# Performance work log

Hardware: AMD Instinct MI355X
Metric: run time of the kernel (lower is better)

The kernel has to match this reference:

```python
import jax, jax.numpy as jnp
import numpy as np

B, T, P, D, V = 8, 4096, 4, 512, 256
N = T // P          # 1024 patches (T divisible by P, so no padding needed)
K = 16              # k_retrieval
W = 4               # local message-passing window
H = 8               # refresh attention heads = min(8, D//64)
ROUNDS = 6
EPS = 1e-5


def layer_norm(x, g, b):
    mu = x.mean(-1, keepdims=True)
    var = ((x - mu) ** 2).mean(-1, keepdims=True)
    return (x - mu) / jnp.sqrt(var + EPS) * g + b


def setup_inputs() -> dict:
    key = jax.random.key(0)
    ks = iter(jax.random.split(key, 48))
    w = lambda *s: jax.random.normal(next(ks), s, jnp.float32) * 0.02
    p = {}
    p['x'] = jax.random.randint(next(ks), (B, T), 0, V)
    p['emb'] = w(V, D)
    p['pos_emb'] = w(P, D)
    p['gru_w_ih'] = w(D, 3 * D); p['gru_w_hh'] = w(D, 3 * D)
    p['gru_b_ih'] = jnp.zeros(3 * D); p['gru_b_hh'] = jnp.zeros(3 * D)
    p['patch_ln_g'] = jnp.ones(D); p['patch_ln_b'] = jnp.zeros(D)
    p['summ_w'] = w(D, D); p['summ_b'] = jnp.zeros(D)
    p['msg_w1'] = w(2 * D, D); p['msg_b1'] = jnp.zeros(D)
    p['msg_w2'] = w(D, D); p['msg_b2'] = jnp.zeros(D)
    p['msg_ln_g'] = jnp.ones(D); p['msg_ln_b'] = jnp.zeros(D)
    p['q_w'] = w(D, D); p['q_b'] = jnp.zeros(D)
    p['k_w'] = w(D, D); p['k_b'] = jnp.zeros(D)
    p['v_w'] = w(D, D); p['v_b'] = jnp.zeros(D)
    p['o_w'] = w(D, D); p['o_b'] = jnp.zeros(D)
    p['gc_w_ih'] = w(2 * D, 3 * D); p['gc_w_hh'] = w(D, 3 * D)
    p['gc_b_ih'] = jnp.zeros(3 * D); p['gc_b_hh'] = jnp.zeros(3 * D)
    p['ar_ln_g'] = jnp.ones(D); p['ar_ln_b'] = jnp.zeros(D)
    p['ar_qkv_w'] = w(D, 3 * D); p['ar_qkv_b'] = jnp.zeros(3 * D)
    p['ar_out_w'] = w(D, D); p['ar_out_b'] = jnp.zeros(D)
    p['broad_w'] = w(D, D); p['broad_b'] = jnp.zeros(D)
    p['ln_g'] = jnp.ones(D); p['ln_b'] = jnp.zeros(D)
    p['head_w'] = w(D, V)
    return p


def reference(x, emb, pos_emb, gru_w_ih, gru_w_hh, gru_b_ih, gru_b_hh,
              patch_ln_g, patch_ln_b, summ_w, summ_b,
              msg_w1, msg_b1, msg_w2, msg_b2, msg_ln_g, msg_ln_b,
              q_w, q_b, k_w, k_b, v_w, v_b, o_w, o_b,
              gc_w_ih, gc_w_hh, gc_b_ih, gc_b_hh,
              ar_ln_g, ar_ln_b, ar_qkv_w, ar_qkv_b, ar_out_w, ar_out_b,
              broad_w, broad_b, ln_g, ln_b, head_w):
    # --- patch encoding: embedding + pos + GRU over the P tokens of each patch ---
    flat = x.reshape(B * N, P)
    h = emb[flat] + pos_emb[None, :, :]                      # [B*N, P, D]

    def gru_step(hprev, xt):
        gi = xt @ gru_w_ih + gru_b_ih
        gh = hprev @ gru_w_hh + gru_b_hh
        ir, iz, inn = jnp.split(gi, 3, -1)
        hr, hz, hn = jnp.split(gh, 3, -1)
        r = jax.nn.sigmoid(ir + hr)
        z = jax.nn.sigmoid(iz + hz)
        n = jnp.tanh(inn + r * hn)
        hnew = (1 - z) * n + z * hprev
        return hnew, hnew

    _, hs = jax.lax.scan(gru_step, jnp.zeros((B * N, D), h.dtype), jnp.swapaxes(h, 0, 1))
    local = layer_norm(jnp.swapaxes(hs, 0, 1), patch_ln_g, patch_ln_b).reshape(B, N, P, D)
    h = local.mean(2) @ summ_w + summ_b                      # patch summaries [B, N, D]

    # --- RoPE tables over patch positions ---
    d = D // 2
    inv_freq = 1.0 / (10000.0 ** (jnp.arange(0, D, 2, dtype=jnp.float32) / D))
    freqs = jnp.arange(N, dtype=jnp.float32)[:, None] * inv_freq[None, :]   # [N, d]
    cos, sin = jnp.cos(freqs), jnp.sin(freqs)

    def rotary(t):
        t1, t2 = t[..., :d], t[..., d:]
        return jnp.concatenate([t1 * cos - t2 * sin, t2 * cos + t1 * sin], -1)

    causal = jnp.tril(jnp.ones((N, N), bool))
    hd = D // H

    for rnd in range(ROUNDS):
        # windowed neighbor gather (W past patches + self), fused MLP messages
        padded = jnp.pad(h, ((0, 0), (W, 0), (0, 0)))
        neighbors = jnp.stack([padded[:, W - w:W - w + N] for w in range(W + 1)], 2)  # [B,N,W+1,D]
        self_exp = jnp.broadcast_to(h[:, :, None, :], neighbors.shape)
        msg_in = jnp.concatenate([self_exp, neighbors], -1)
        msgs = (jax.nn.gelu(msg_in @ msg_w1 + msg_b1, approximate=False) @ msg_w2 + msg_b2).mean(2)

        # RoPE top-k sparse causal attention (N > K, sparse branch always taken)
        q = rotary(h @ q_w + q_b)
        k = rotary(h @ k_w + k_b)
        v = h @ v_w + v_b
        scores = jnp.einsum('bnd,bmd->bnm', q, k) / jnp.sqrt(jnp.float32(D))
        scores = jnp.where(causal, scores, -jnp.inf)
        tv, ti = jax.lax.top_k(scores, K)
        probs = jax.nn.softmax(tv, -1)  # == softmax of -inf-filled sparse score matrix
        vg = jax.vmap(lambda vi, ii: vi[ii])(v, ti)          # [B, N, K, D]
        retrieved = jnp.einsum('bnk,bnkd->bnd', probs, vg) @ o_w + o_b

        # GRUCell gated write
        wi = jnp.concatenate([msgs, retrieved], -1)
        gi = wi @ gc_w_ih + gc_b_ih
        gh = h @ gc_w_hh + gc_b_hh
        ir, iz, inn = jnp.split(gi, 3, -1)
        hr, hz, hn = jnp.split(gh, 3, -1)
        r = jax.nn.sigmoid(ir + hr)
        z = jax.nn.sigmoid(iz + hz)
        n = jnp.tanh(inn + r * hn)
        h = layer_norm((1 - z) * n + z * h, msg_ln_g, msg_ln_b)

        # global causal MHA refresh every 2 rounds (eval mode, no dropout)
        if (rnd + 1) % 2 == 0:
            res = h
            hn_ = layer_norm(h, ar_ln_g, ar_ln_b)
            qkv = hn_ @ ar_qkv_w + ar_qkv_b
            qh, kh, vh = [t.reshape(B, N, H, hd) for t in jnp.split(qkv, 3, -1)]
            s = jnp.einsum('bnhd,bmhd->bhnm', qh, kh) / jnp.sqrt(jnp.float32(hd))
            a = jax.nn.softmax(jnp.where(causal, s, -jnp.inf), -1)
            o = jnp.einsum('bhnm,bmhd->bnhd', a, vh).reshape(B, N, D)
            h = res + (o @ ar_out_w + ar_out_b)

    # broadcast patch state back to tokens, project to vocab
    broad = h @ broad_w + broad_b
    final = (local + broad[:, :, None, :]).reshape(B, N * P, D)[:, :T]
    return layer_norm(final, ln_g, ln_b) @ head_w            # [B, T, V]
```

## Files before the change

### kernel.cpp

```cpp
#include <hip/hip_runtime.h>
#include <math.h>

constexpr int CB = 8, CT = 4096, CP = 4, CD = 512, CV = 256;
constexpr int CN = 1024, CK = 16, CH = 8, CHD = 64;
constexpr int ROWS = CB * CN;
constexpr int TROWS = CB * CT;
constexpr float CEPS = 1e-5f;
constexpr size_t PN = (size_t)ROWS * CD;

constexpr size_t OFF_LOCAL = 0;
constexpr size_t OFF_HP    = OFF_LOCAL + (size_t)ROWS * CP * CD;
constexpr size_t OFF_X4    = OFF_HP    + PN;
constexpr size_t OFF_MS    = OFF_X4    + (size_t)ROWS * 2560;
constexpr size_t OFF_A     = OFF_MS    + PN;
constexpr size_t OFF_B     = OFF_A     + PN;
constexpr size_t OFF_BIAS  = OFF_B     + PN;
constexpr size_t OFF_WT    = OFF_BIAS  + 4096;

constexpr size_t TOT_W    = 7471104;
constexpr size_t T_GRU_IH = 0;
constexpr size_t T_GRU_HH = 786432;
constexpr size_t T_SUMM   = 1572864;
constexpr size_t T_FUSE   = 1835008;
constexpr size_t T_MSG2   = 3145728;
constexpr size_t T_OW     = 3407872;
constexpr size_t T_GCAB   = 3670016;
constexpr size_t T_GC_HH  = 5242880;
constexpr size_t T_AR_QKV = 6029312;
constexpr size_t T_AR_OUT = 6815744;
constexpr size_t T_BROAD  = 7077888;
constexpr size_t T_HEAD   = 7340032;

constexpr int F_ACC_F32  = 1;
constexpr int F_ACC_PAIR = 2;
constexpr int F_WR_F32   = 4;
constexpr int F_WR_PAIR  = 8;
constexpr int F_TRI      = 16;
constexpr int F_SPLIT    = 32;

typedef __attribute__((ext_vector_type(8))) short short8;
typedef __attribute__((ext_vector_type(4))) float f32x4;

__device__ __forceinline__ float sigm(float x) { return 1.f / (1.f + expf(-x)); }
__device__ __forceinline__ float geluf(float x) {
  return 0.5f * x * (1.f + erff(x * 0.7071067811865475f));
}
__device__ __forceinline__ unsigned short bf_hi(float x) {
  const unsigned u = __float_as_uint(x);
  return (unsigned short)((u + 0x7FFFu + ((u >> 16) & 1u)) >> 16);
}
__device__ __forceinline__ float bf_f(unsigned short h) {
  return __uint_as_float((unsigned)h << 16);
}
__device__ __forceinline__ void split_store(float v, unsigned short* ph, unsigned short* pl) {
  const unsigned short h = bf_hi(v);
  *ph = h; *pl = bf_hi(v - bf_f(h));
}
__device__ __forceinline__ float blk_sum(float v, float* red) {
#pragma unroll
  for (int o = 32; o > 0; o >>= 1) v += __shfl_down(v, o, 64);
  const int wv = threadIdx.x >> 6, ln = threadIdx.x & 63;
  __syncthreads();
  if (ln == 0) red[wv] = v;
  __syncthreads();
  return red[0] + red[1] + red[2] + red[3];
}

__device__ __forceinline__ int xcd_swz(int i, int n) {
  if (n < 8) return i;
  const int q = n >> 3, r = n & 7;
  const int xcd = i & 7, slot = i >> 3;
  return (xcd < r ? xcd * (q + 1) : r * (q + 1) + (xcd - r) * q) + slot;
}

__global__ __launch_bounds__(256) void transpose_split(const float* __restrict__ in,
                                                       unsigned short* __restrict__ oh,
                                                       unsigned short* __restrict__ ol,
                                                       int K, int N, int ldk, int ko)
{
  __shared__ float tile[32][33];
  const int n0 = blockIdx.x * 32, k0 = blockIdx.y * 32;
  const int tx = threadIdx.x & 31, ty = threadIdx.x >> 5;
#pragma unroll
  for (int i = 0; i < 32; i += 8)
    tile[ty + i][tx] = in[(size_t)(k0 + ty + i) * N + n0 + tx];
  __syncthreads();
#pragma unroll
  for (int i = 0; i < 32; i += 8) {
    const float v = tile[tx][ty + i];
    const unsigned short h = bf_hi(v);
    const size_t o = (size_t)(n0 + ty + i) * ldk + ko + k0 + tx;
    oh[o] = h;
    ol[o] = bf_hi(v - bf_f(h));
  }
}

__global__ void concat_bias5(const float* __restrict__ b1, const float* __restrict__ qb,
                             const float* __restrict__ kb, const float* __restrict__ vb,
                             float* __restrict__ o)
{
  const int i = blockIdx.x * 256 + threadIdx.x;
  float v;
  if (i < 512) v = b1[i];
  else if (i < 1024) v = 0.f;
  else if (i < 1536) v = qb[i - 1024];
  else if (i < 2048) v = kb[i - 1536];
  else v = vb[i - 2048];
  o[i] = v;
}

template <bool P3>
__global__ __launch_bounds__(256, 2) void gemm_bf3(
    const unsigned short* __restrict__ AH, const unsigned short* __restrict__ AL,
    const unsigned short* __restrict__ A2H, const unsigned short* __restrict__ A2L,
    int K1, int lda,
    const unsigned short* __restrict__ BH, const unsigned short* __restrict__ BL, int ldb,
    const float* __restrict__ bias, float scale,
    float* __restrict__ Cf, int ldc, float* __restrict__ Cf2,
    unsigned short* __restrict__ CHp, unsigned short* __restrict__ CLp, int ldcp,
    int K, int flags, long long sA, long long sB, long long sC)
{
  AH += (size_t)blockIdx.z * sA; AL += (size_t)blockIdx.z * sA;
  BH += (size_t)blockIdx.z * sB; BL += (size_t)blockIdx.z * sB;
  if (Cf) Cf += (size_t)blockIdx.z * sC;
  int bm, bn;
  if (flags & F_TRI) {
    int t = xcd_swz(blockIdx.x, gridDim.x), i = 0, acc = 0;
    while (acc + i + 1 <= t) { ++i; acc += i; }
    bm = i << 7; bn = (t - acc) << 7;
  } else {
    const int w = xcd_swz(blockIdx.x + gridDim.x * blockIdx.y, gridDim.x * gridDim.y);
    bm = (w / gridDim.x) << 7; bn = (w % gridDim.x) << 7;
  }
  __shared__ __align__(16) unsigned short AsH[128][40];
  __shared__ __align__(16) unsigned short AsL[128][40];
  __shared__ __align__(16) unsigned short BsH[128][40];
  __shared__ __align__(16) unsigned short BsL[P3 ? 128 : 1][40];
  const int tid = threadIdx.x;
  const int lane = tid & 63, wave = tid >> 6;
  const int wm = (wave & 1) << 6, wn = (wave >> 1) << 6;
  const int r16 = lane & 15, quad = lane >> 4;
  const int sr = tid >> 1, sc = (tid & 1) << 4;
  const f32x4 zero = {0.f, 0.f, 0.f, 0.f};
  f32x4 acc[4][4];
#pragma unroll
  for (int i = 0; i < 4; ++i)
#pragma unroll
    for (int j = 0; j < 4; ++j) acc[i][j] = zero;

  for (int k0 = 0; k0 < K; k0 += 32) {
    const int kc = k0 + sc;
    const unsigned short *pAH, *pAL;
    if (kc < K1) {
      pAH = AH + (size_t)(bm + sr) * lda + kc;
      pAL = AL + (size_t)(bm + sr) * lda + kc;
    } else {
      pAH = A2H + (size_t)(bm + sr) * lda + (kc - K1);
      pAL = A2L + (size_t)(bm + sr) * lda + (kc - K1);
    }
    const unsigned short* pBH = BH + (size_t)(bn + sr) * ldb + kc;
    *(uint4*)&AsH[sr][sc]     = *(const uint4*)pAH;
    *(uint4*)&AsH[sr][sc + 8] = *(const uint4*)(pAH + 8);
    *(uint4*)&AsL[sr][sc]     = *(const uint4*)pAL;
    *(uint4*)&AsL[sr][sc + 8] = *(const uint4*)(pAL + 8);
    *(uint4*)&BsH[sr][sc]     = *(const uint4*)pBH;
    *(uint4*)&BsH[sr][sc + 8] = *(const uint4*)(pBH + 8);
    if (P3) {
      const unsigned short* pBL = BL + (size_t)(bn + sr) * ldb + kc;
      *(uint4*)&BsL[sr][sc]     = *(const uint4*)pBL;
      *(uint4*)&BsL[sr][sc + 8] = *(const uint4*)(pBL + 8);
    }
    __syncthreads();
    short8 bh[4], bl[4];
#pragma unroll
    for (int ni = 0; ni < 4; ++ni) {
      bh[ni] = *(const short8*)&BsH[wn + ni * 16 + r16][quad * 8];
      if (P3) bl[ni] = *(const short8*)&BsL[wn + ni * 16 + r16][quad * 8];
    }
#pragma unroll
    for (int mi = 0; mi < 4; ++mi) {
      const short8 ah = *(const short8*)&AsH[wm + mi * 16 + r16][quad * 8];
      const short8 al = *(const short8*)&AsL[wm + mi * 16 + r16][quad * 8];
#pragma unroll
      for (int ni = 0; ni < 4; ++ni) {
        acc[mi][ni] = __builtin_amdgcn_mfma_f32_16x16x32_bf16(ah, bh[ni], acc[mi][ni], 0, 0, 0);
        acc[mi][ni] = __builtin_amdgcn_mfma_f32_16x16x32_bf16(al, bh[ni], acc[mi][ni], 0, 0, 0);
        if (P3)
          acc[mi][ni] = __builtin_amdgcn_mfma_f32_16x16x32_bf16(ah, bl[ni], acc[mi][ni], 0, 0, 0);
      }
    }
    __syncthreads();
  }
#pragma unroll
  for (int mi = 0; mi < 4; ++mi) {
    const int row0 = bm + wm + mi * 16 + quad * 4;
#pragma unroll
    for (int ni = 0; ni < 4; ++ni) {
      const int col = bn + wn + ni * 16 + r16;
      const float bv = bias ? bias[col] : 0.f;
#pragma unroll
      for (int rg = 0; rg < 4; ++rg) {
        const int row = row0 + rg;
        float o = acc[mi][ni][rg] * scale + bv;
        if (flags & F_SPLIT) {
          if (col < 1024) {
            float* p = Cf + (size_t)row * ldc + col;
            *p = o + *p;
          } else {
            Cf2[(size_t)row * 512 + (col - 1024)] = o;
          }
        } else {
          if (flags & F_ACC_F32) o += Cf[(size_t)row * ldc + col];
          if (flags & F_ACC_PAIR) {
            const size_t ip = (size_t)row * ldcp + col;
            o += bf_f(CHp[ip]) + bf_f(CLp[ip]);
          }
          if (flags & F_WR_F32) Cf[(size_t)row * ldc + col] = o;
          if (flags & F_WR_PAIR) {
            const size_t ip = (size_t)row * ldcp + col;
            split_store(o, &CHp[ip], &CLp[ip]);
          }
        }
      }
    }
  }
}

__global__ __launch_bounds__(256, 3) void gemm_bf3s(
    const unsigned short* __restrict__ AH, const unsigned short* __restrict__ AL, int lda,
    const unsigned short* __restrict__ BH, int ldb,
    const float* __restrict__ bias,
    float* __restrict__ Cf, int ldc,
    unsigned short* __restrict__ CHp, unsigned short* __restrict__ CLp, int ldcp,
    int K, int flags)
{
  const int w = xcd_swz(blockIdx.x + gridDim.x * blockIdx.y, gridDim.x * gridDim.y);
  const int bm = (w / gridDim.x) << 6, bn = (w % gridDim.x) << 7;
  __shared__ __align__(16) unsigned short AsH[64][40];
  __shared__ __align__(16) unsigned short AsL[64][40];
  __shared__ __align__(16) unsigned short BsH[128][40];
  const int tid = threadIdx.x;
  const int lane = tid & 63, wave = tid >> 6;
  const int wm = (wave & 1) << 5, wn = (wave >> 1) << 6;
  const int r16 = lane & 15, quad = lane >> 4;
  const int sar = tid >> 2, sac = (tid & 3) << 3;
  const int sbr = tid >> 1, sbc = (tid & 1) << 4;
  const f32x4 zero = {0.f, 0.f, 0.f, 0.f};
  f32x4 acc[2][4];
#pragma unroll
  for (int i = 0; i < 2; ++i)
#pragma unroll
    for (int j = 0; j < 4; ++j) acc[i][j] = zero;

  for (int k0 = 0; k0 < K; k0 += 32) {
    const unsigned short* pAH = AH + (size_t)(bm + sar) * lda + k0 + sac;
    const unsigned short* pAL = AL + (size_t)(bm + sar) * lda + k0 + sac;
    const unsigned short* pBH = BH + (size_t)(bn + sbr) * ldb + k0 + sbc;
    *(uint4*)&AsH[sar][sac] = *(const uint4*)pAH;
    *(uint4*)&AsL[sar][sac] = *(const uint4*)pAL;
    *(uint4*)&BsH[sbr][sbc]     = *(const uint4*)pBH;
    *(uint4*)&BsH[sbr][sbc + 8] = *(const uint4*)(pBH + 8);
    __syncthreads();
    short8 bh[4];
#pragma unroll
    for (int ni = 0; ni < 4; ++ni)
      bh[ni] = *(const short8*)&BsH[wn + ni * 16 + r16][quad * 8];
#pragma unroll
    for (int mi = 0; mi < 2; ++mi) {
      const short8 ah = *(const short8*)&AsH[wm + mi * 16 + r16][quad * 8];
      const short8 al = *(const short8*)&AsL[wm + mi * 16 + r16][quad * 8];
#pragma unroll
      for (int ni = 0; ni < 4; ++ni) {
        acc[mi][ni] = __builtin_amdgcn_mfma_f32_16x16x32_bf16(ah, bh[ni], acc[mi][ni], 0, 0, 0);
        acc[mi][ni] = __builtin_amdgcn_mfma_f32_16x16x32_bf16(al, bh[ni], acc[mi][ni], 0, 0, 0);
      }
    }
    __syncthreads();
  }
#pragma unroll
  for (int mi = 0; mi < 2; ++mi) {
    const int row0 = bm + wm + mi * 16 + quad * 4;
#pragma unroll
    for (int ni = 0; ni < 4; ++ni) {
      const int col = bn + wn + ni * 16 + r16;
      const float bv = bias ? bias[col] : 0.f;
#pragma unroll
      for (int rg = 0; rg < 4; ++rg) {
        const int row = row0 + rg;
        float o = acc[mi][ni][rg] + bv;
        if (flags & F_ACC_PAIR) {
          const size_t ip = (size_t)row * ldcp + col;
          o += bf_f(CHp[ip]) + bf_f(CLp[ip]);
        }
        if (flags & F_WR_F32) Cf[(size_t)row * ldc + col] = o;
        if (flags & F_WR_PAIR) {
          const size_t ip = (size_t)row * ldcp + col;
          split_store(o, &CHp[ip], &CLp[ip]);
        }
      }
    }
  }
}

__global__ void zero_k(float* __restrict__ p) {
  p[(size_t)blockIdx.x * 256 + threadIdx.x] = 0.f;
}

__global__ void embed_p(const int* __restrict__ x, const float* __restrict__ emb,
                        const float* __restrict__ pos,
                        unsigned short* __restrict__ oh, unsigned short* __restrict__ ol, int t)
{
  const int i = blockIdx.x * 256 + threadIdx.x;
  const int r = i >> 9, d = i & 511;
  const int b = r >> 10, n = r & (CN - 1);
  const int tok = x[b * CT + n * CP + t];
  const float v = emb[(size_t)tok * CD + d] + pos[t * CD + d];
  split_store(v, &oh[i], &ol[i]);
}

__global__ void gru_point_p(const float* __restrict__ gi, const float* __restrict__ ghn,
                            unsigned short* __restrict__ hH, unsigned short* __restrict__ hL,
                            float* __restrict__ hs, int t)
{
  const int i = blockIdx.x * 256 + threadIdx.x;
  const int r = i >> 9, d = i & 511;
  const size_t gb = (size_t)r * (3 * CD) + d;
  const float sr_ = gi[gb], sz = gi[gb + CD], inn = gi[gb + 2 * CD];
  const float hn = ghn[i];
  const float hp = bf_f(hH[i]) + bf_f(hL[i]);
  const float rr = sigm(sr_), zz = sigm(sz);
  const float nn = tanhf(inn + rr * hn);
  const float hv = (1.f - zz) * nn + zz * hp;
  split_store(hv, &hH[i], &hL[i]);
  hs[(size_t)r * (CP * CD) + (size_t)t * CD + d] = hv;
}

__global__ __launch_bounds__(256) void ln_rows(const float* __restrict__ in, float* __restrict__ out,
                                               const float* __restrict__ g, const float* __restrict__ b)
{
  const int r = blockIdx.x, t = threadIdx.x;
  __shared__ float red[4];
  const float* ip = in + (size_t)r * CD;
  const float v0 = ip[t], v1 = ip[t + 256];
  const float mu = blk_sum(v0 + v1, red) * (1.f / CD);
  const float d0 = v0 - mu, d1 = v1 - mu;
  const float var = blk_sum(d0 * d0 + d1 * d1, red) * (1.f / CD);
  const float inv = rsqrtf(var + CEPS);
  float* op = out + (size_t)r * CD;
  op[t] = d0 * inv * g[t] + b[t];
  op[t + 256] = d1 * inv * g[t + 256] + b[t + 256];
}

__global__ void mean_pool_p(const float* __restrict__ local,
                            unsigned short* __restrict__ oh, unsigned short* __restrict__ ol)
{
  const int i = blockIdx.x * 256 + threadIdx.x;
  const int r = i >> 9, d = i & 511;
  const float* p = local + (size_t)r * (CP * CD) + d;
  split_store(0.25f * (p[0] + p[CD] + p[2 * CD] + p[3 * CD]), &oh[i], &ol[i]);
}

__global__ void msg_gelu_p(const float* __restrict__ X4,
                           unsigned short* __restrict__ oh, unsigned short* __restrict__ ol)
{
  const int i = blockIdx.x * 256 + threadIdx.x;
  const int r = i >> 9, d = i & 511;
  const int n = r & (CN - 1);
  const float pv = X4[(size_t)r * 2560 + d];
  float acc = 0.f;
#pragma unroll
  for (int w = 0; w <= 4; ++w) {
    const float xv = pv + ((n >= w) ? X4[(size_t)(r - w) * 2560 + 512 + d] : 0.f);
    acc += geluf(xv);
  }
  split_store(acc * 0.2f, &oh[i], &ol[i]);
}

__global__ void rotary2_p(const float* __restrict__ X4,
                          unsigned short* __restrict__ qh, unsigned short* __restrict__ ql,
                          unsigned short* __restrict__ kh, unsigned short* __restrict__ kl)
{
  const int i = blockIdx.x * 256 + threadIdx.x;
  const int r = i >> 8, j = i & 255;
  const int n = r & (CN - 1);
  const float fr = (float)n * expf(-9.210340371976184f * ((float)j * (1.f / 256.f)));
  float s, c;
  sincosf(fr, &s, &c);
  const float* p = X4 + (size_t)r * 2560;
  const size_t o0 = (size_t)r * CD + j, o1 = o0 + 256;
  const float q1 = p[1024 + j], q2 = p[1024 + 256 + j];
  split_store(q1 * c - q2 * s, &qh[o0], &ql[o0]);
  split_store(q2 * c + q1 * s, &qh[o1], &ql[o1]);
  const float k1 = p[1536 + j], k2 = p[1536 + 256 + j];
  split_store(k1 * c - k2 * s, &kh[o0], &kl[o0]);
  split_store(k2 * c + k1 * s, &kh[o1], &kl[o1]);
}

__global__ __launch_bounds__(256) void topk_attn(const float* __restrict__ X4,
                                                 unsigned short* __restrict__ ctxH,
                                                 unsigned short* __restrict__ ctxL)
{
  const int r = xcd_swz(blockIdx.x, gridDim.x);
  const int b = r >> 10, n = r & (CN - 1);
  const float* row = X4 + (size_t)r * 2560;
  const int tid = threadIdx.x, lane = tid & 63, wave = tid >> 6;
  __shared__ unsigned long long cands[64];
  __shared__ float p16[CK];
  __shared__ int i16[CK];
  unsigned long long key[4];
#pragma unroll
  for (int q = 0; q < 4; ++q) {
    const int m = tid + q * 256;
    const float v = (m <= n) ? row[m] : -INFINITY;
    unsigned u = __float_as_uint(v);
    u = (u & 0x80000000u) ? ~u : (u | 0x80000000u);
    key[q] = ((unsigned long long)u << 32) | (unsigned)(CN - 1 - m);
  }
  unsigned long long mycand = 0ull;
#pragma unroll
  for (int it = 0; it < CK; ++it) {
    unsigned long long best = key[0];
#pragma unroll
    for (int q = 1; q < 4; ++q) best = best > key[q] ? best : key[q];
#pragma unroll
    for (int o = 32; o > 0; o >>= 1) {
      const unsigned long long o2 = __shfl_xor(best, o, 64);
      best = best > o2 ? best : o2;
    }
    if (lane == it) mycand = best;
#pragma unroll
    for (int q = 0; q < 4; ++q)
      if (key[q] == best) key[q] = 0ull;
  }
  if (lane < CK) cands[wave * CK + lane] = mycand;
  __syncthreads();
  if (wave == 0) {
    unsigned long long k2 = cands[lane];
    unsigned long long mine = 0ull;
#pragma unroll
    for (int it = 0; it < CK; ++it) {
      unsigned long long best = k2;
#pragma unroll
      for (int o = 32; o > 0; o >>= 1) {
        const unsigned long long o2 = __shfl_xor(best, o, 64);
        best = best > o2 ? best : o2;
      }
      if (lane == it) mine = best;
      if (k2 == best) k2 = 0ull;
    }
    unsigned u = (unsigned)(mine >> 32);
    u = (u & 0x80000000u) ? (u & 0x7FFFFFFFu) : ~u;
    const float val = __uint_as_float(u);
    const int idx = CN - 1 - (int)(mine & 0xFFFFFFFFu);
    const float mx = __shfl(val, 0, 64);
    float e = 0.f;
    if (lane < CK && val != -INFINITY) e = expf(val - mx);
    float sum = e;
#pragma unroll
    for (int o = 32; o > 0; o >>= 1) sum += __shfl_xor(sum, o, 64);
    if (lane < CK) {
      p16[lane] = e / sum;
      i16[lane] = idx;
    }
  }
  __syncthreads();
  const size_t vb = ((size_t)b << 10);
#pragma unroll
  for (int pass = 0; pass < 2; ++pass) {
    const int d = tid + pass * 256;
    float a = 0.f;
#pragma unroll
    for (int q = 0; q < CK; ++q)
      a += p16[q] * X4[(vb + i16[q]) * 2560 + 2048 + d];
    split_store(a, &ctxH[(size_t)r * CD + d], &ctxL[(size_t)r * CD + d]);
  }
}

__global__ __launch_bounds__(256) void gru_ln_p(const float* __restrict__ gi, const float* __restrict__ ghn,
                                                unsigned short* __restrict__ hH, unsigned short* __restrict__ hL,
                                                const float* __restrict__ g, const float* __restrict__ b,
                                                unsigned short* __restrict__ aH, unsigned short* __restrict__ aL,
                                                const float* __restrict__ g2, const float* __restrict__ b2)
{
  const int r = blockIdx.x, t = threadIdx.x;
  __shared__ float red[4];
  float u[2];
#pragma unroll
  for (int q = 0; q < 2; ++q) {
    const int d = t + q * 256;
    const size_t gb = (size_t)r * (3 * CD) + d;
    const float sr_ = gi[gb], sz = gi[gb + CD], inn = gi[gb + 2 * CD];
    const float hn = ghn[(size_t)r * CD + d];
    const size_t hi = (size_t)r * CD + d;
    const float hp = bf_f(hH[hi]) + bf_f(hL[hi]);
    const float rr = sigm(sr_), zz = sigm(sz);
    const float nn = tanhf(inn + rr * hn);
    u[q] = (1.f - zz) * nn + zz * hp;
  }
  const float mu = blk_sum(u[0] + u[1], red) * (1.f / CD);
  const float d0 = u[0] - mu, d1 = u[1] - mu;
  const float var = blk_sum(d0 * d0 + d1 * d1, red) * (1.f / CD);
  const float inv = rsqrtf(var + CEPS);
  const float h0 = d0 * inv * g[t] + b[t];
  const float h1 = d1 * inv * g[t + 256] + b[t + 256];
  split_store(h0, &hH[(size_t)r * CD + t], &hL[(size_t)r * CD + t]);
  split_store(h1, &hH[(size_t)r * CD + t + 256], &hL[(size_t)r * CD + t + 256]);
  if (aH) {
    const float mu2 = blk_sum(h0 + h1, red) * (1.f / CD);
    const float e0 = h0 - mu2, e1 = h1 - mu2;
    const float var2 = blk_sum(e0 * e0 + e1 * e1, red) * (1.f / CD);
    const float inv2 = rsqrtf(var2 + CEPS);
    split_store(e0 * inv2 * g2[t] + b2[t], &aH[(size_t)r * CD + t], &aL[(size_t)r * CD + t]);
    split_store(e1 * inv2 * g2[t + 256] + b2[t + 256],
                &aH[(size_t)r * CD + t + 256], &aL[(size_t)r * CD + t + 256]);
  }
}

constexpr int FP = 72;
__global__ __launch_bounds__(256, 2) void flash_attn_p(const unsigned short* __restrict__ qkvH,
                                                       const unsigned short* __restrict__ qkvL,
                                                       unsigned short* __restrict__ outH,
                                                       unsigned short* __restrict__ outL)
{
  __shared__ __align__(16) unsigned short Qh[64 * FP], Ql[64 * FP];
  __shared__ __align__(16) unsigned short Kh[64 * FP], Kl[64 * FP];
  __shared__ __align__(16) unsigned short Vth[64 * FP], Vtl[64 * FP];
  __shared__ __align__(16) unsigned short Pm[64 * FP];
  const int w = xcd_swz(blockIdx.x, gridDim.x);
  const int qt = w & 15, head = (w >> 4) & 7, b = w >> 7;
  const int tid = threadIdx.x;
  const int lane = tid & 63, wave = tid >> 6;
  const int r16 = lane & 15, quad = lane >> 4;
  const size_t base = (size_t)b * CN * (3 * CD) + head * CHD;

  {
    const int r = tid >> 2, c0 = (tid & 3) << 4;
    const unsigned short* qh = qkvH + base + (size_t)(qt * 64 + r) * (3 * CD) + c0;
    const unsigned short* ql = qkvL + base + (size_t)(qt * 64 + r) * (3 * CD) + c0;
    *(uint4*)&Qh[r * FP + c0]     = *(const uint4*)qh;
    *(uint4*)&Qh[r * FP + c0 + 8] = *(const uint4*)(qh + 8);
    *(uint4*)&Ql[r * FP + c0]     = *(const uint4*)ql;
    *(uint4*)&Ql[r * FP + c0 + 8] = *(const uint4*)(ql + 8);
  }
  float m_i[4], l_i[4];
  f32x4 O[4];
  const f32x4 zero = {0.f, 0.f, 0.f, 0.f};
#pragma unroll
  for (int r = 0; r < 4; ++r) { m_i[r] = -INFINITY; l_i[r] = 0.f; }
#pragma unroll
  for (int d = 0; d < 4; ++d) O[d] = zero;

  const int skr = tid >> 2, skc = (tid & 3) << 4;
  const int rp = (tid >> 3) << 1, c0v = (tid & 7) << 3;
  const unsigned short* kbH = qkvH + base + CD;
  const unsigned short* kbL = qkvL + base + CD;
  const unsigned short* vbH = qkvH + base + 2 * CD;
  const unsigned short* vbL = qkvL + base + 2 * CD;

  uint4 kh0, kh1, kl0, kl1, vxh, vyh, vxl, vyl;
  auto LOADJ = [&](int j) {
    const size_t ko = (size_t)(j * 64 + skr) * (3 * CD) + skc;
    kh0 = *(const uint4*)(kbH + ko);
    kh1 = *(const uint4*)(kbH + ko + 8);
    kl0 = *(const uint4*)(kbL + ko);
    kl1 = *(const uint4*)(kbL + ko + 8);
    const size_t vo = (size_t)(j * 64 + rp) * (3 * CD) + c0v;
    vxh = *(const uint4*)(vbH + vo);
    vyh = *(const uint4*)(vbH + vo + 3 * CD);
    vxl = *(const uint4*)(vbL + vo);
    vyl = *(const uint4*)(vbL + vo + 3 * CD);
  };

  LOADJ(0);
  for (int j = 0; j <= qt; ++j) {
    *(uint4*)&Kh[skr * FP + skc]     = kh0;
    *(uint4*)&Kh[skr * FP + skc + 8] = kh1;
    *(uint4*)&Kl[skr * FP + skc]     = kl0;
    *(uint4*)&Kl[skr * FP + skc + 8] = kl1;
    {
      unsigned short xh[8], yh[8], xl[8], yl[8];
      *(uint4*)xh = vxh; *(uint4*)yh = vyh;
      *(uint4*)xl = vxl; *(uint4*)yl = vyl;
#pragma unroll
      for (int c = 0; c < 8; ++c) {
        const int R = c0v + c;
        const int col = rp ^ ((R >> 3) << 3);
        *(unsigned*)&Vth[R * FP + col] = (unsigned)xh[c] | ((unsigned)yh[c] << 16);
        *(unsigned*)&Vtl[R * FP + col] = (unsigned)xl[c] | ((unsigned)yl[c] << 16);
      }
    }
    __syncthreads();
    if (j < qt) LOADJ(j + 1);
    f32x4 S[4];
#pragma unroll
    for (int nt = 0; nt < 4; ++nt) S[nt] = zero;
#pragma unroll
    for (int kh2 = 0; kh2 < 2; ++kh2) {
      const short8 qh = *(const short8*)&Qh[(wave * 16 + r16) * FP + kh2 * 32 + quad * 8];
      const short8 ql = *(const short8*)&Ql[(wave * 16 + r16) * FP + kh2 * 32 + quad * 8];
#pragma unroll
      for (int nt = 0; nt < 4; ++nt) {
        const short8 kkh = *(const short8*)&Kh[(nt * 16 + r16) * FP + kh2 * 32 + quad * 8];
        const short8 kkl = *(const short8*)&Kl[(nt * 16 + r16) * FP + kh2 * 32 + quad * 8];
        S[nt] = __builtin_amdgcn_mfma_f32_16x16x32_bf16(qh, kkh, S[nt], 0, 0, 0);
        S[nt] = __builtin_amdgcn_mfma_f32_16x16x32_bf16(qh, kkl, S[nt], 0, 0, 0);
        S[nt] = __builtin_amdgcn_mfma_f32_16x16x32_bf16(ql, kkh, S[nt], 0, 0, 0);
      }
    }
#pragma unroll
    for (int r = 0; r < 4; ++r) {
      const int qrow = wave * 16 + quad * 4 + r;
      float s[4];
#pragma unroll
      for (int nt = 0; nt < 4; ++nt) {
        s[nt] = S[nt][r] * 0.125f;
        if (j == qt && (nt * 16 + r16) > qrow) s[nt] = -1e30f;
      }
      float rm = fmaxf(fmaxf(s[0], s[1]), fmaxf(s[2], s[3]));
#pragma unroll
      for (int o = 8; o > 0; o >>= 1) rm = fmaxf(rm, __shfl_xor(rm, o, 64));
      const float newm = fmaxf(m_i[r], rm);
      float p[4], rs = 0.f;
#pragma unroll
      for (int nt = 0; nt < 4; ++nt) { p[nt] = expf(s[nt] - newm); rs += p[nt]; }
#pragma unroll
      for (int o = 8; o > 0; o >>= 1) rs += __shfl_xor(rs, o, 64);
      const float alpha = expf(m_i[r] - newm);
      l_i[r] = l_i[r] * alpha + rs;
      m_i[r] = newm;
#pragma unroll
      for (int dt = 0; dt < 4; ++dt) O[dt][r] *= alpha;
#pragma unroll
      for (int nt = 0; nt < 4; ++nt)
        Pm[qrow * FP + nt * 16 + r16] = bf_hi(p[nt]);
    }
    __syncthreads();
#pragma unroll
    for (int kh2 = 0; kh2 < 2; ++kh2) {
      const short8 pa = *(const short8*)&Pm[(wave * 16 + r16) * FP + kh2 * 32 + quad * 8];
#pragma unroll
      for (int dt = 0; dt < 4; ++dt) {
        const int R = dt * 16 + r16;
        const int col = (kh2 * 32 + quad * 8) ^ ((R >> 3) << 3);
        const short8 vh = *(const short8*)&Vth[R * FP + col];
        const short8 vl = *(const short8*)&Vtl[R * FP + col];
        O[dt] = __builtin_amdgcn_mfma_f32_16x16x32_bf16(pa, vh, O[dt], 0, 0, 0);
        O[dt] = __builtin_amdgcn_mfma_f32_16x16x32_bf16(pa, vl, O[dt], 0, 0, 0);
      }
    }
    __syncthreads();
  }
#pragma unroll
  for (int r = 0; r < 4; ++r) {
    const float inv = 1.f / l_i[r];
    const size_t row = (size_t)b * CN + qt * 64 + wave * 16 + quad * 4 + r;
#pragma unroll
    for (int dt = 0; dt < 4; ++dt) {
      const size_t o = row * CD + head * CHD + dt * 16 + r16;
      split_store(O[dt][r] * inv, &outH[o], &outL[o]);
    }
  }
}

__global__ __launch_bounds__(256) void final_ln_p(const float* __restrict__ local,
                                                  const float* __restrict__ broad,
                                                  const float* __restrict__ g, const float* __restrict__ bb,
                                                  unsigned short* __restrict__ oh,
                                                  unsigned short* __restrict__ ol)
{
  const int r = blockIdx.x, t = threadIdx.x;
  __shared__ float red[4];
  const size_t lb = (size_t)r * CD;
  const size_t br = (size_t)(r >> 2) * CD;
  const float v0 = local[lb + t] + broad[br + t];
  const float v1 = local[lb + 256 + t] + broad[br + 256 + t];
  const float mu = blk_sum(v0 + v1, red) * (1.f / CD);
  const float d0 = v0 - mu, d1 = v1 - mu;
  const float var = blk_sum(d0 * d0 + d1 * d1, red) * (1.f / CD);
  const float inv = rsqrtf(var + CEPS);
  split_store(d0 * inv * g[t] + bb[t], &oh[lb + t], &ol[lb + t]);
  split_store(d1 * inv * g[t + 256] + bb[t + 256], &oh[lb + 256 + t], &ol[lb + 256 + t]);
}

extern "C" void kernel_launch(void* const* d_in, const int* in_sizes, int n_in,
                              void* d_out, int out_size, void* d_ws, size_t ws_size,
                              hipStream_t stream)
{
  (void)in_sizes; (void)n_in; (void)out_size; (void)ws_size;
  const int*   x         = (const int*)d_in[0];
  const float* emb       = (const float*)d_in[1];
  const float* pos_emb   = (const float*)d_in[2];
  const float* gru_w_ih  = (const float*)d_in[3];
  const float* gru_w_hh  = (const float*)d_in[4];
  const float* gru_b_ih  = (const float*)d_in[5];
  const float* gru_b_hh  = (const float*)d_in[6];
  const float* patch_g   = (const float*)d_in[7];
  const float* patch_b   = (const float*)d_in[8];
  const float* summ_w    = (const float*)d_in[9];
  const float* summ_b    = (const float*)d_in[10];
  const float* msg_w1    = (const float*)d_in[11];
  const float* msg_b1    = (const float*)d_in[12];
  const float* msg_w2    = (const float*)d_in[13];
  const float* msg_b2    = (const float*)d_in[14];
  const float* msg_ln_g  = (const float*)d_in[15];
  const float* msg_ln_b  = (const float*)d_in[16];
  const float* q_w       = (const float*)d_in[17];
  const float* q_b       = (const float*)d_in[18];
  const float* k_w       = (const float*)d_in[19];
  const float* k_b       = (const float*)d_in[20];
  const float* v_w       = (const float*)d_in[21];
  const float* v_b       = (const float*)d_in[22];
  const float* o_w       = (const float*)d_in[23];
  const float* o_b       = (const float*)d_in[24];
  const float* gc_w_ih   = (const float*)d_in[25];
  const float* gc_w_hh   = (const float*)d_in[26];
  const float* gc_b_ih   = (const float*)d_in[27];
  const float* gc_b_hh   = (const float*)d_in[28];
  const float* ar_ln_g   = (const float*)d_in[29];
  const float* ar_ln_b   = (const float*)d_in[30];
  const float* ar_qkv_w  = (const float*)d_in[31];
  const float* ar_qkv_b  = (const float*)d_in[32];
  const float* ar_out_w  = (const float*)d_in[33];
  const float* ar_out_b  = (const float*)d_in[34];
  const float* broad_w   = (const float*)d_in[35];
  const float* broad_b   = (const float*)d_in[36];
  const float* ln_g      = (const float*)d_in[37];
  const float* ln_b      = (const float*)d_in[38];
  const float* head_w    = (const float*)d_in[39];
  float* out = (float*)d_out;

  float* ws = (float*)d_ws;
  float* WL    = ws + OFF_LOCAL;
  float* X4    = ws + OFF_X4;
  float* GI    = X4;
  float* GHN   = X4 + (size_t)ROWS * 1536;
  float* WBR   = ws + OFF_MS;
  float* Wbias5 = ws + OFF_BIAS;
  unsigned short* WTh = (unsigned short*)(ws + OFF_WT);
  unsigned short* WTl = WTh + TOT_W;
  unsigned short* WhH = (unsigned short*)(ws + OFF_HP);
  unsigned short* WhL = WhH + PN;
  unsigned short* MsH = (unsigned short*)(ws + OFF_MS);
  unsigned short* MsL = MsH + PN;
  unsigned short* pAH = (unsigned short*)(ws + OFF_A);
  unsigned short* pAL = pAH + PN;
  unsigned short* pBH = (unsigned short*)(ws + OFF_B);
  unsigned short* pBL = pBH + PN;
  unsigned short* QkH = (unsigned short*)X4;
  unsigned short* QkL = QkH + (size_t)ROWS * 1536;
  unsigned short* FnH = (unsigned short*)X4;
  unsigned short* FnL = FnH + (size_t)TROWS * CD;

  const int EW = ROWS * CD / 256;
  const float inv_sqrt_d = 0.04419417382415922f;

  auto TR = [&](const float* in, size_t off, int K, int N, int ldk, int ko) {
    transpose_split<<<dim3(N / 32, K / 32), 256, 0, stream>>>(in, WTh + off, WTl + off, K, N, ldk, ko);
  };
  TR(gru_w_ih, T_GRU_IH, 512, 1536, 512, 0);
  TR(gru_w_hh, T_GRU_HH, 512, 1536, 512, 0);
  TR(summ_w,   T_SUMM,   512, 512,  512, 0);
  TR(msg_w1,                      T_FUSE,           512, 512, 512, 0);
  TR(msg_w1 + (size_t)512 * 512,  T_FUSE + 262144,  512, 512, 512, 0);
  TR(q_w,                         T_FUSE + 524288,  512, 512, 512, 0);
  TR(k_w,                         T_FUSE + 786432,  512, 512, 512, 0);
  TR(v_w,                         T_FUSE + 1048576, 512, 512, 512, 0);
  TR(msg_w2,   T_MSG2,   512, 512,  512, 0);
  TR(o_w, T_OW, 512, 512, 512, 0);
  TR(gc_w_ih,                       T_GCAB, 512, 1536, 1024, 0);
  TR(gc_w_ih + (size_t)512 * 1536,  T_GCAB, 512, 1536, 1024, 512);
  TR(gc_w_hh,  T_GC_HH,  512, 1536, 512, 0);
  TR(ar_qkv_w, T_AR_QKV, 512, 1536, 512, 0);
  TR(ar_out_w, T_AR_OUT, 512, 512,  512, 0);
  TR(broad_w,  T_BROAD,  512, 512,  512, 0);
  TR(head_w,   T_HEAD,   512, 256,  512, 0);
  concat_bias5<<<10, 256, 0, stream>>>(msg_b1, q_b, k_b, v_b, Wbias5);

  auto G3 = [&](const unsigned short* AH_, const unsigned short* AL_, int lda_,
                size_t toff, int ldb_, const float* bias_, float* Cf_, int ldc_, float* Cf2_,
                unsigned short* CHp_, unsigned short* CLp_, int ldcp_,
                int K_, int flags_, int gx, int gy) {
    gemm_bf3<false><<<dim3(gx, gy), 256, 0, stream>>>(
        AH_, AL_, AH_, AL_, K_, lda_, WTh + toff, WTl + toff, ldb_, bias_, 1.f,
        Cf_, ldc_, Cf2_, CHp_, CLp_, ldcp_, K_, flags_, 0, 0, 0);
  };
  auto G3S = [&](const unsigned short* AH_, const unsigned short* AL_, int lda_,
                 size_t toff, const float* bias_, float* Cf_, int ldc_,
                 unsigned short* CHp_, unsigned short* CLp_, int ldcp_,
                 int flags_, int gx, int gy) {
    gemm_bf3s<<<dim3(gx, gy), 256, 0, stream>>>(
        AH_, AL_, lda_, WTh + toff, 512, bias_,
        Cf_, ldc_, CHp_, CLp_, ldcp_, 512, flags_);
  };

  zero_k<<<EW, 256, 0, stream>>>(ws + OFF_HP);
  for (int t = 0; t < CP; ++t) {
    embed_p<<<EW, 256, 0, stream>>>(x, emb, pos_emb, pAH, pAL, t);
    G3(pAH, pAL, 512, T_GRU_IH, 512, gru_b_ih, GI, 1536, nullptr,
       nullptr, nullptr, 0, 512, F_WR_F32, 12, 64);
    G3(WhH, WhL, 512, T_GRU_HH, 512, gru_b_hh, GI, 1536, GHN,
       nullptr, nullptr, 0, 512, F_SPLIT, 12, 64);
    gru_point_p<<<EW, 256, 0, stream>>>(GI, GHN, WhH, WhL, WL, t);
  }
  ln_rows<<<TROWS, 256, 0, stream>>>(WL, WL, patch_g, patch_b);
  mean_pool_p<<<EW, 256, 0, stream>>>(WL, pAH, pAL);
  G3S(pAH, pAL, 512, T_SUMM, summ_b, nullptr, 0, WhH, WhL, 512, F_WR_PAIR, 4, 128);

  for (int rnd = 0; rnd < 6; ++rnd) {
    G3(WhH, WhL, 512, T_FUSE, 512, Wbias5, X4, 2560, nullptr,
       nullptr, nullptr, 0, 512, F_WR_F32, 20, 64);
    msg_gelu_p<<<EW, 256, 0, stream>>>(X4, pBH, pBL);
    G3S(pBH, pBL, 512, T_MSG2, msg_b2, nullptr, 0, MsH, MsL, 512, F_WR_PAIR, 4, 128);
    rotary2_p<<<ROWS, 256, 0, stream>>>(X4, pAH, pAL, pBH, pBL);
    gemm_bf3<true><<<dim3(36, 1, CB), 256, 0, stream>>>(
        pAH, pAL, pAH, pAL, 512, 512, pBH, pBL, 512, nullptr, inv_sqrt_d,
        X4, 2560, nullptr, nullptr, nullptr, 0, 512, F_WR_F32 | F_TRI,
        (long long)CN * CD, (long long)CN * CD, (long long)CN * 2560);
    topk_attn<<<ROWS, 256, 0, stream>>>(X4, pAH, pAL);
    G3S(pAH, pAL, 512, T_OW, o_b, nullptr, 0, pBH, pBL, 512, F_WR_PAIR, 4, 128);
    gemm_bf3<false><<<dim3(12, 64), 256, 0, stream>>>(
        MsH, MsL, pBH, pBL, 512, 512, WTh + T_GCAB, WTl + T_GCAB, 1024, gc_b_ih, 1.f,
        GI, 1536, nullptr, nullptr, nullptr, 0, 1024, F_WR_F32, 0, 0, 0);
    G3(WhH, WhL, 512, T_GC_HH, 512, gc_b_hh, GI, 1536, GHN,
       nullptr, nullptr, 0, 512, F_SPLIT, 12, 64);
    if ((rnd & 1) == 1) {
      gru_ln_p<<<ROWS, 256, 0, stream>>>(GI, GHN, WhH, WhL, msg_ln_g, msg_ln_b,
                                         pAH, pAL, ar_ln_g, ar_ln_b);
      G3(pAH, pAL, 512, T_AR_QKV, 512, ar_qkv_b, nullptr, 0, nullptr,
         QkH, QkL, 1536, 512, F_WR_PAIR, 12, 64);
      flash_attn_p<<<dim3(16 * CH * CB), 256, 0, stream>>>(QkH, QkL, pBH, pBL);
      G3S(pBH, pBL, 512, T_AR_OUT, ar_out_b, nullptr, 0, WhH, WhL, 512,
          F_ACC_PAIR | F_WR_PAIR, 4, 128);
    } else {
      gru_ln_p<<<ROWS, 256, 0, stream>>>(GI, GHN, WhH, WhL, msg_ln_g, msg_ln_b,
                                         nullptr, nullptr, nullptr, nullptr);
    }
  }

  G3S(WhH, WhL, 512, T_BROAD, broad_b, WBR, 512, nullptr, nullptr, 0, F_WR_F32, 4, 128);
  final_ln_p<<<TROWS, 256, 0, stream>>>(WL, WBR, ln_g, ln_b, FnH, FnL);
  G3S(FnH, FnL, 512, T_HEAD, nullptr, out, CV, nullptr, nullptr, 0, F_WR_F32, 2, 512);
}
```

Baseline: 3.794 ms.

## Process one top-k attention row per wavefront instead of per block

The top-k retrieval kernel now assigns one row to each 64-lane wave, four rows per block, removing the block-wide candidate merge and both __syncthreads barriers. Each lane holds 16 keys and caches its own running maximum, recomputing it only when its element wins a round, which cuts per-iteration compare work. The value gather is hoisted into per-lane probability and offset registers. The cost is higher register pressure from the 16 64-bit keys and a launch of a quarter as many blocks.

```diff
diff --git a/kernel.cpp b/kernel.cpp
--- a/kernel.cpp
+++ b/kernel.cpp
@@ -400,78 +400,87 @@
                                                  unsigned short* __restrict__ ctxH,
                                                  unsigned short* __restrict__ ctxL)
 {
-  const int r = xcd_swz(blockIdx.x, gridDim.x);
+  const int g = xcd_swz(blockIdx.x, gridDim.x);
+  const int wave = threadIdx.x >> 6, lane = threadIdx.x & 63;
+  const int r = g * 4 + wave;
   const int b = r >> 10, n = r & (CN - 1);
   const float* row = X4 + (size_t)r * 2560;
-  const int tid = threadIdx.x, lane = tid & 63, wave = tid >> 6;
-  __shared__ unsigned long long cands[64];
-  __shared__ float p16[CK];
-  __shared__ int i16[CK];
-  unsigned long long key[4];
-#pragma unroll
-  for (int q = 0; q < 4; ++q) {
-    const int m = tid + q * 256;
+  __shared__ float p16s[4][CK];
+  __shared__ int   i16s[4][CK];
+
+  unsigned long long key[16];
+#pragma unroll
+  for (int q = 0; q < 16; ++q) {
+    const int m = q * 64 + lane;
     const float v = (m <= n) ? row[m] : -INFINITY;
     unsigned u = __float_as_uint(v);
     u = (u & 0x80000000u) ? ~u : (u | 0x80000000u);
     key[q] = ((unsigned long long)u << 32) | (unsigned)(CN - 1 - m);
   }
-  unsigned long long mycand = 0ull;
+  unsigned long long lane_best;
+  {
+    unsigned long long t[8];
+#pragma unroll
+    for (int i = 0; i < 8; ++i) t[i] = key[i] > key[i + 8] ? key[i] : key[i + 8];
+#pragma unroll
+    for (int i = 0; i < 4; ++i) t[i] = t[i] > t[i + 4] ? t[i] : t[i + 4];
+    t[0] = t[0] > t[2] ? t[0] : t[2];
+    t[1] = t[1] > t[3] ? t[1] : t[3];
+    lane_best = t[0] > t[1] ? t[0] : t[1];
+  }
+  unsigned long long mine = 0ull;
 #pragma unroll
   for (int it = 0; it < CK; ++it) {
-    unsigned long long best = key[0];
-#pragma unroll
-    for (int q = 1; q < 4; ++q) best = best > key[q] ? best : key[q];
+    unsigned long long best = lane_best;
 #pragma unroll
     for (int o = 32; o > 0; o >>= 1) {
       const unsigned long long o2 = __shfl_xor(best, o, 64);
       best = best > o2 ? best : o2;
     }
-    if (lane == it) mycand = best;
-#pragma unroll
-    for (int q = 0; q < 4; ++q)
-      if (key[q] == best) key[q] = 0ull;
-  }
-  if (lane < CK) cands[wave * CK + lane] = mycand;
-  __syncthreads();
-  if (wave == 0) {
-    unsigned long long k2 = cands[lane];
-    unsigned long long mine = 0ull;
-#pragma unroll
-    for (int it = 0; it < CK; ++it) {
-      unsigned long long best = k2;
-#pragma unroll
-      for (int o = 32; o > 0; o >>= 1) {
-        const unsigned long long o2 = __shfl_xor(best, o, 64);
-        best = best > o2 ? best : o2;
-      }
-      if (lane == it) mine = best;
-      if (k2 == best) k2 = 0ull;
-    }
-    unsigned u = (unsigned)(mine >> 32);
-    u = (u & 0x80000000u) ? (u & 0x7FFFFFFFu) : ~u;
-    const float val = __uint_as_float(u);
-    const int idx = CN - 1 - (int)(mine & 0xFFFFFFFFu);
-    const float mx = __shfl(val, 0, 64);
-    float e = 0.f;
-    if (lane < CK && val != -INFINITY) e = expf(val - mx);
-    float sum = e;
-#pragma unroll
-    for (int o = 32; o > 0; o >>= 1) sum += __shfl_xor(sum, o, 64);
-    if (lane < CK) {
-      p16[lane] = e / sum;
-      i16[lane] = idx;
-    }
-  }
-  __syncthreads();
-  const size_t vb = ((size_t)b << 10);
-#pragma unroll
-  for (int pass = 0; pass < 2; ++pass) {
-    const int d = tid + pass * 256;
+    if (lane == it) mine = best;
+    if (lane_best == best) {
+#pragma unroll
+      for (int q = 0; q < 16; ++q)
+        if (key[q] == best) key[q] = 0ull;
+      unsigned long long t[8];
+#pragma unroll
+      for (int i = 0; i < 8; ++i) t[i] = key[i] > key[i + 8] ? key[i] : key[i + 8];
+#pragma unroll
+      for (int i = 0; i < 4; ++i) t[i] = t[i] > t[i + 4] ? t[i] : t[i + 4];
+      t[0] = t[0] > t[2] ? t[0] : t[2];
+      t[1] = t[1] > t[3] ? t[1] : t[3];
+      lane_best = t[0] > t[1] ? t[0] : t[1];
+    }
+  }
+  unsigned u = (unsigned)(mine >> 32);
+  u = (u & 0x80000000u) ? (u & 0x7FFFFFFFu) : ~u;
+  const float val = __uint_as_float(u);
+  const int idx = CN - 1 - (int)(mine & 0xFFFFFFFFu);
+  const float mx = __shfl(val, 0, 64);
+  float e = 0.f;
+  if (lane < CK && val != -INFINITY) e = expf(val - mx);
+  float sum = e;
+#pragma unroll
+  for (int o = 8; o > 0; o >>= 1) sum += __shfl_xor(sum, o, 64);
+  if (lane < CK) {
+    p16s[wave][lane] = e / sum;
+    i16s[wave][lane] = idx;
+  }
+  float pr[CK];
+  int   ro[CK];
+  const int vb = b << 10;
+#pragma unroll
+  for (int q = 0; q < CK; ++q) {
+    pr[q] = p16s[wave][q];
+    ro[q] = (vb + i16s[wave][q]) * 2560 + 2048;
+  }
+#pragma unroll
+  for (int pass = 0; pass < 8; ++pass) {
+    const int d = pass * 64 + lane;
     float a = 0.f;
 #pragma unroll
     for (int q = 0; q < CK; ++q)
-      a += p16[q] * X4[(vb + i16[q]) * 2560 + 2048 + d];
+      a += pr[q] * X4[(size_t)ro[q] + d];
     split_store(a, &ctxH[(size_t)r * CD + d], &ctxL[(size_t)r * CD + d]);
   }
 }
@@ -816,7 +825,7 @@
         pAH, pAL, pAH, pAL, 512, 512, pBH, pBL, 512, nullptr, inv_sqrt_d,
         X4, 2560, nullptr, nullptr, nullptr, 0, 512, F_WR_F32 | F_TRI,
         (long long)CN * CD, (long long)CN * CD, (long long)CN * 2560);
-    topk_attn<<<ROWS, 256, 0, stream>>>(X4, pAH, pAL);
+    topk_attn<<<ROWS / 4, 256, 0, stream>>>(X4, pAH, pAL);
     G3S(pAH, pAL, 512, T_OW, o_b, nullptr, 0, pBH, pBL, 512, F_WR_PAIR, 4, 128);
     gemm_bf3<false><<<dim3(12, 64), 256, 0, stream>>>(
         MsH, MsL, pBH, pBL, 512, 512, WTh + T_GCAB, WTl + T_GCAB, 1024, gc_b_ih, 1.f,
```

Result: faster. 3.619 ms (-4.6%).
